# Kernel optimization log

Hardware: AMD Instinct MI355X
Metric: run time of the kernel (lower is better)

The kernel has to match this reference:

```python
import jax, jax.numpy as jnp
import numpy as np

N_NODES = 25000
N_EDGES = 400000
ATOM_DIM = 39
EDGE_DIM = 10
FP = 128


def setup_inputs() -> dict:
    key = jax.random.key(0)
    ks = iter(jax.random.split(key, 40))
    def rn(shape, scale=0.1):
        return (jax.random.normal(next(ks), shape, dtype=jnp.float32) * scale)
    inp = {
        'x': jax.random.normal(next(ks), (N_NODES, ATOM_DIM), dtype=jnp.float32),
        'edge_index': jax.random.randint(next(ks), (2, N_EDGES), 0, N_NODES, dtype=jnp.int32),
        'edge_attr': jax.random.normal(next(ks), (N_EDGES, EDGE_DIM), dtype=jnp.float32),
        # layer 0 (step=0): atom_fc + neighbor_fc + align/attend/GRU
        'l0_atom_fc_w': rn((FP, ATOM_DIM)), 'l0_atom_fc_b': rn((FP,)),
        'l0_neighbor_fc_w': rn((FP, ATOM_DIM + EDGE_DIM)), 'l0_neighbor_fc_b': rn((FP,)),
        'l0_align_w': rn((1, 2 * FP)), 'l0_align_b': rn((1,)),
        'l0_attend_w': rn((FP, FP)), 'l0_attend_b': rn((FP,)),
        'l0_w_ih': rn((3 * FP, FP)), 'l0_w_hh': rn((3 * FP, FP)),
        'l0_b_ih': rn((3 * FP,)), 'l0_b_hh': rn((3 * FP,)),
        # layer 1 (step=1): align/attend/GRU only
        'l1_align_w': rn((1, 2 * FP)), 'l1_align_b': rn((1,)),
        'l1_attend_w': rn((FP, FP)), 'l1_attend_b': rn((FP,)),
        'l1_w_ih': rn((3 * FP, FP)), 'l1_w_hh': rn((3 * FP, FP)),
        'l1_b_ih': rn((3 * FP,)), 'l1_b_hh': rn((3 * FP,)),
    }
    return inp


def _lrelu(v):
    return jax.nn.leaky_relu(v, negative_slope=0.01)


def _gru_cell(inp, h, w_ih, w_hh, b_ih, b_hh):
    # torch.nn.GRUCell math
    gi = inp @ w_ih.T + b_ih
    gh = h @ w_hh.T + b_hh
    i_r, i_z, i_n = jnp.split(gi, 3, axis=-1)
    h_r, h_z, h_n = jnp.split(gh, 3, axis=-1)
    r = jax.nn.sigmoid(i_r + h_r)
    z = jax.nn.sigmoid(i_z + h_z)
    n = jnp.tanh(i_n + r * h_n)
    return (1.0 - z) * n + z * h


def _segment_softmax(e, idx, num_segments):
    # PyG torch_geometric.utils.softmax: per-segment max-shifted exp / (sum + 1e-16)
    m = jax.ops.segment_max(e, idx, num_segments=num_segments)
    ex = jnp.exp(e - m[idx])
    s = jax.ops.segment_sum(ex, idx, num_segments=num_segments)
    return ex / (s[idx] + 1e-16)


def _edge_block(x_i, x_j, src, dst, n_nodes, aw, ab, tw, tb, w_ih, w_hh, b_ih, b_hh):
    # align -> segment softmax (keyed by source index, as in the torch code) -> attend -> GRU -> scatter-add
    evu = _lrelu(jnp.concatenate([x_i, x_j], axis=-1) @ aw.T + ab)      # [E,1]
    avu = _segment_softmax(evu, src, n_nodes)                            # [E,1]
    c = jax.nn.elu(avu * (x_i @ tw.T + tb))                              # [E,FP]; dropout is identity in eval
    h = _gru_cell(c, x_i, w_ih, w_hh, b_ih, b_hh)                        # [E,FP]
    return jax.ops.segment_sum(h, dst, num_segments=n_nodes)            # [N,FP] default 'add' aggregation


def reference(x, edge_index, edge_attr,
              l0_atom_fc_w, l0_atom_fc_b, l0_neighbor_fc_w, l0_neighbor_fc_b,
              l0_align_w, l0_align_b, l0_attend_w, l0_attend_b,
              l0_w_ih, l0_w_hh, l0_b_ih, l0_b_hh,
              l1_align_w, l1_align_b, l1_attend_w, l1_attend_b,
              l1_w_ih, l1_w_hh, l1_b_ih, l1_b_hh):
    src, dst = edge_index[0], edge_index[1]   # PyG flow source_to_target: x_j=x[src], x_i=x[dst]
    n_nodes = x.shape[0]
    # --- layer 0 (step == 0) ---
    x_i = _lrelu(x[dst] @ l0_atom_fc_w.T + l0_atom_fc_b)
    x_j = _lrelu(jnp.concatenate([x[src], edge_attr], axis=-1) @ l0_neighbor_fc_w.T + l0_neighbor_fc_b)
    x = _edge_block(x_i, x_j, src, dst, n_nodes,
                    l0_align_w, l0_align_b, l0_attend_w, l0_attend_b,
                    l0_w_ih, l0_w_hh, l0_b_ih, l0_b_hh)
    # --- layer 1 (step == 1) ---
    x_i = x[dst]
    x_j = x[src]
    x = _edge_block(x_i, x_j, src, dst, n_nodes,
                    l1_align_w, l1_align_b, l1_attend_w, l1_attend_b,
                    l1_w_ih, l1_w_hh, l1_b_ih, l1_b_hh)
    return x
```

## Files before the change

kernel.cpp:

```cpp
#include <hip/hip_runtime.h>
#include <math.h>

#define NN 25000
#define NE 400000
#define NINF -1e30f

typedef __attribute__((ext_vector_type(8))) short bf16x8;
typedef __attribute__((ext_vector_type(4))) float f32x4;

__device__ __forceinline__ float lrelu(float x){ return x > 0.f ? x : 0.01f*x; }
__device__ __forceinline__ float elu1(float x){ return x > 0.f ? x : (__expf(x)-1.f); }
__device__ __forceinline__ float sigm(float x){ return 1.f/(1.f+__expf(-x)); }
__device__ __forceinline__ float tanh_fast(float x){ float e=__expf(2.f*x); return 1.f - 2.f/(e+1.f); }
__device__ __forceinline__ short f2bf(float f){
    union { float f; unsigned u; } v; v.f = f;
    unsigned r = v.u + 0x7fff + ((v.u >> 16) & 1);
    return (short)(r >> 16);
}
__device__ __forceinline__ float bf2f(short s){
    union { unsigned u; float f; } v; v.u = ((unsigned)(unsigned short)s) << 16;
    return v.f;
}

__global__ __launch_bounds__(256) void k_pack6(
    const float* __restrict__ w0, const float* __restrict__ w1,
    const float* __restrict__ w2, const float* __restrict__ w3,
    const float* __restrict__ w4, const float* __restrict__ w5,
    short* __restrict__ o0, short* __restrict__ o1, short* __restrict__ o2,
    short* __restrict__ o3, short* __restrict__ o4, short* __restrict__ o5)
{
    int b = blockIdx.x;
    const float* w; short* o; int idx;
    if      (b < 192){ w=w0; o=o0; idx = b*256; }
    else if (b < 384){ w=w1; o=o1; idx = (b-192)*256; }
    else if (b < 576){ w=w2; o=o2; idx = (b-384)*256; }
    else if (b < 768){ w=w3; o=o3; idx = (b-576)*256; }
    else if (b < 832){ w=w4; o=o4; idx = (b-768)*256; }
    else             { w=w5; o=o5; idx = (b-832)*256; }
    idx += threadIdx.x;
    int i    = idx & 7;
    int lane = (idx >> 3) & 63;
    int ks   = (idx >> 9) & 3;
    int tile = idx >> 11;
    int row  = tile*16 + (lane & 15);
    int k    = ks*32 + ((lane >> 4) << 3) + i;
    o[idx] = f2bf(w[row*128 + k]);
}

__global__ __launch_bounds__(256) void k_hist2(const int* __restrict__ src,
                                               const int* __restrict__ dst,
                                               unsigned* __restrict__ hd,
                                               unsigned* __restrict__ hs)
{
    int e = blockIdx.x*256 + threadIdx.x;
    if (e < NE){
        atomicAdd(&hd[dst[e]], 1u);
        atomicAdd(&hs[src[e]], 1u);
    }
}

__global__ __launch_bounds__(1024) void k_scan2(
    const unsigned* __restrict__ hd, unsigned* __restrict__ cd,
    const unsigned* __restrict__ hs, unsigned* __restrict__ cs,
    int* __restrict__ srcptr)
{
    __shared__ unsigned ps[1024];
    const int issrc = blockIdx.x;
    const unsigned* h = issrc ? hs : hd;
    unsigned* c = issrc ? cs : cd;
    const int t = threadIdx.x;
    unsigned loc[25]; unsigned sum = 0;
    const int base = t*25;
    #pragma unroll
    for (int i=0;i<25;i++){ int n=base+i; unsigned v=(n<NN)?h[n]:0u; loc[i]=sum; sum+=v; }
    ps[t]=sum; __syncthreads();
    for (int off=1; off<1024; off<<=1){
        unsigned v = (t>=off)? ps[t-off] : 0u;
        __syncthreads();
        ps[t] += v;
        __syncthreads();
    }
    unsigned bex = (t==0)? 0u : ps[t-1];
    #pragma unroll
    for (int i=0;i<25;i++){
        int n=base+i;
        if (n<NN){
            unsigned off = bex + loc[i];
            c[n] = off;
            if (issrc) srcptr[n] = (int)off;
        }
    }
    if (issrc && t==1023) srcptr[NN] = NE;
}

__global__ __launch_bounds__(256) void k_scatter2(
    const int* __restrict__ src, const int* __restrict__ dst,
    unsigned* __restrict__ cd, unsigned* __restrict__ cs,
    int* __restrict__ se_dst, int* __restrict__ inv_dst,
    int* __restrict__ se2_id, int* __restrict__ se2_dst)
{
    int e = blockIdx.x*256 + threadIdx.x;
    if (e < NE){
        int d = dst[e], s = src[e];
        unsigned p = atomicAdd(&cd[d], 1u);
        se_dst[p] = d;
        inv_dst[e] = (int)p;
        unsigned q = atomicAdd(&cs[s], 1u);
        se2_id[q] = e;
        se2_dst[q] = d;
    }
}

__global__ __launch_bounds__(256) void k_l0_node(
    const float* __restrict__ x,
    const float* __restrict__ wa, const float* __restrict__ ba,
    const float* __restrict__ wn, const float* __restrict__ bn,
    const float* __restrict__ aw,
    short* __restrict__ A16, short* __restrict__ B16, float* __restrict__ di)
{
    __shared__ float xs[32][40];
    __shared__ float As[32][130];
    const int t = threadIdx.x;
    const int base = blockIdx.x * 32;
    for (int idx = t; idx < 32*39; idx += 256){
        int nn = idx / 39, k = idx - nn*39;
        int node = base + nn;
        xs[nn][k] = (node < NN) ? x[(size_t)node*39 + k] : 0.f;
    }
    __syncthreads();
    const int j = t & 127;
    const int g = t >> 7;
    {
        float accA[16], accB[16];
        #pragma unroll
        for (int nn=0; nn<16; ++nn){ accA[nn]=0.f; accB[nn]=0.f; }
        for (int k=0; k<39; ++k){
            float wva = wa[j*39+k];
            float wvb = wn[j*49+k];
            #pragma unroll
            for (int nn=0; nn<16; ++nn){
                float xv = xs[g*16+nn][k];
                accA[nn] += xv*wva;
                accB[nn] += xv*wvb;
            }
        }
        float bav = ba[j], bnv = bn[j];
        #pragma unroll
        for (int nn=0; nn<16; ++nn){
            int node = base + g*16 + nn;
            float av = lrelu(accA[nn] + bav);
            As[g*16+nn][j] = av;
            if (node < NN){
                A16[(size_t)node*128 + j] = f2bf(av);
                B16[(size_t)node*128 + j] = f2bf(accB[nn] + bnv);
            }
        }
    }
    __syncthreads();
    if (t < 32){
        int node = base + t;
        if (node < NN){
            float d = 0.f;
            for (int k=0; k<128; ++k) d += As[t][k]*aw[k];
            di[node] = d;
        }
    }
}

__global__ __launch_bounds__(512) void k_node_prep(
    const short* __restrict__ A16,
    const short* __restrict__ twp, const float* __restrict__ tb,
    const short* __restrict__ whhp, const float* __restrict__ bhh,
    short* __restrict__ T16, short* __restrict__ GH16)
{
    __shared__ __align__(16) char A_lds[64*272];
    const int t = threadIdx.x;
    const int base = blockIdx.x << 6;
    #pragma unroll
    for (int it=0; it<2; ++it){
        int cid = it*512 + t;
        int row = cid >> 4, ch = cid & 15;
        int node = base + row; if (node >= NN) node = NN-1;
        *(int4*)(A_lds + row*272 + ch*16) = *(const int4*)(A16 + (size_t)node*128 + ch*8);
    }
    __syncthreads();
    const int w = t >> 6, lane = t & 63;
    const int l15 = lane & 15, lhi = lane >> 4;
    const int jb = w*16 + l15;
    f32x4 Tacc[4], gh[4][3];
    {
        float tbv = tb[jb];
        #pragma unroll
        for (int m=0; m<4; ++m) Tacc[m] = (f32x4){tbv, tbv, tbv, tbv};
        #pragma unroll
        for (int g=0; g<3; ++g){
            float bv = bhh[g*128 + jb];
            #pragma unroll
            for (int m=0; m<4; ++m) gh[m][g] = (f32x4){bv, bv, bv, bv};
        }
    }
    #pragma unroll
    for (int ks=0; ks<4; ++ks){
        bf16x8 af[4];
        #pragma unroll
        for (int m=0; m<4; ++m)
            af[m] = *(const bf16x8*)(A_lds + (m*16+l15)*272 + ks*64 + (lhi<<4));
        bf16x8 tf = *(const bf16x8*)(twp + (size_t)((w*4 + ks)*64 + lane)*8);
        #pragma unroll
        for (int m=0; m<4; ++m)
            Tacc[m] = __builtin_amdgcn_mfma_f32_16x16x32_bf16(af[m], tf, Tacc[m], 0, 0, 0);
        #pragma unroll
        for (int g=0; g<3; ++g){
            bf16x8 wf = *(const bf16x8*)(whhp + (size_t)(((g*8+w)*4 + ks)*64 + lane)*8);
            #pragma unroll
            for (int m=0; m<4; ++m)
                gh[m][g] = __builtin_amdgcn_mfma_f32_16x16x32_bf16(af[m], wf, gh[m][g], 0, 0, 0);
        }
    }
    #pragma unroll
    for (int m=0; m<4; ++m){
        #pragma unroll
        for (int reg=0; reg<4; ++reg){
            int node = base + m*16 + lhi*4 + reg;
            if (node < NN){
                T16[(size_t)node*128 + jb]        = f2bf(Tacc[m][reg]);
                GH16[(size_t)node*384 + jb]       = f2bf(gh[m][0][reg]);
                GH16[(size_t)node*384 + 128 + jb] = f2bf(gh[m][1][reg]);
                GH16[(size_t)node*384 + 256 + jb] = f2bf(gh[m][2][reg]);
            }
        }
    }
}

__global__ __launch_bounds__(512) void k_l1_prep(
    const float* __restrict__ out0, const float* __restrict__ aw,
    const short* __restrict__ twp, const float* __restrict__ tb,
    const short* __restrict__ whhp, const float* __restrict__ bhh,
    short* __restrict__ x16, float* __restrict__ di, float* __restrict__ dj,
    short* __restrict__ T16, short* __restrict__ GH16)
{
    __shared__ __align__(16) char x_lds[64*272];
    const int t = threadIdx.x;
    const int base = blockIdx.x << 6;
    {
        int r = t >> 3, c0 = (t & 7) * 16;
        int node = base + r;
        int nc = node < NN ? node : NN-1;
        const float4* sp = (const float4*)(out0 + (size_t)nc*128 + c0);
        float4 f0 = sp[0], f1 = sp[1], f2 = sp[2], f3 = sp[3];
        union { short s[16]; int4 v[2]; } u;
        u.s[0]=f2bf(f0.x); u.s[1]=f2bf(f0.y); u.s[2]=f2bf(f0.z); u.s[3]=f2bf(f0.w);
        u.s[4]=f2bf(f1.x); u.s[5]=f2bf(f1.y); u.s[6]=f2bf(f1.z); u.s[7]=f2bf(f1.w);
        u.s[8]=f2bf(f2.x); u.s[9]=f2bf(f2.y); u.s[10]=f2bf(f2.z); u.s[11]=f2bf(f2.w);
        u.s[12]=f2bf(f3.x); u.s[13]=f2bf(f3.y); u.s[14]=f2bf(f3.z); u.s[15]=f2bf(f3.w);
        *(int4*)(x_lds + r*272 + c0*2)      = u.v[0];
        *(int4*)(x_lds + r*272 + c0*2 + 16) = u.v[1];
        if (node < NN){
            *(int4*)(x16 + (size_t)node*128 + c0)     = u.v[0];
            *(int4*)(x16 + (size_t)node*128 + c0 + 8) = u.v[1];
        }
    }
    __syncthreads();
    const int w = t >> 6, lane = t & 63;
    {
        float a0 = aw[lane], a1 = aw[64+lane], a2 = aw[128+lane], a3 = aw[192+lane];
        for (int i=0;i<8;++i){
            int r = w*8 + i;
            int node = base + r;
            float v0 = bf2f(*(const short*)(x_lds + r*272 + lane*2));
            float v1 = bf2f(*(const short*)(x_lds + r*272 + 128 + lane*2));
            float pa = v0*a0 + v1*a1;
            float pb = v0*a2 + v1*a3;
            #pragma unroll
            for (int off=32; off; off>>=1){ pa += __shfl_xor(pa,off); pb += __shfl_xor(pb,off); }
            if (lane==0 && node<NN){ di[node]=pa; dj[node]=pb; }
        }
    }
    const int l15 = lane & 15, lhi = lane >> 4;
    const int jb = w*16 + l15;
    f32x4 Tacc[4], gh[4][3];
    {
        float tbv = tb[jb];
        #pragma unroll
        for (int m=0; m<4; ++m) Tacc[m] = (f32x4){tbv, tbv, tbv, tbv};
        #pragma unroll
        for (int g=0; g<3; ++g){
            float bv = bhh[g*128 + jb];
            #pragma unroll
            for (int m=0; m<4; ++m) gh[m][g] = (f32x4){bv, bv, bv, bv};
        }
    }
    #pragma unroll
    for (int ks=0; ks<4; ++ks){
        bf16x8 af[4];
        #pragma unroll
        for (int m=0; m<4; ++m)
            af[m] = *(const bf16x8*)(x_lds + (m*16+l15)*272 + ks*64 + (lhi<<4));
        bf16x8 tf = *(const bf16x8*)(twp + (size_t)((w*4 + ks)*64 + lane)*8);
        #pragma unroll
        for (int m=0; m<4; ++m)
            Tacc[m] = __builtin_amdgcn_mfma_f32_16x16x32_bf16(af[m], tf, Tacc[m], 0, 0, 0);
        #pragma unroll
        for (int g=0; g<3; ++g){
            bf16x8 wf = *(const bf16x8*)(whhp + (size_t)(((g*8+w)*4 + ks)*64 + lane)*8);
            #pragma unroll
            for (int m=0; m<4; ++m)
                gh[m][g] = __builtin_amdgcn_mfma_f32_16x16x32_bf16(af[m], wf, gh[m][g], 0, 0, 0);
        }
    }
    #pragma unroll
    for (int m=0; m<4; ++m){
        #pragma unroll
        for (int reg=0; reg<4; ++reg){
            int node = base + m*16 + lhi*4 + reg;
            if (node < NN){
                T16[(size_t)node*128 + jb]        = f2bf(Tacc[m][reg]);
                GH16[(size_t)node*384 + jb]       = f2bf(gh[m][0][reg]);
                GH16[(size_t)node*384 + 128 + jb] = f2bf(gh[m][1][reg]);
                GH16[(size_t)node*384 + 256 + jb] = f2bf(gh[m][2][reg]);
            }
        }
    }
}

__global__ __launch_bounds__(256) void k_align0(
    const int* __restrict__ srcptr, const int* __restrict__ se2_id,
    const int* __restrict__ se2_dst, const int* __restrict__ inv_dst,
    const float* __restrict__ ea, const short* __restrict__ B16,
    const float* __restrict__ wn, const float* __restrict__ aw,
    const float* __restrict__ ab, const float* __restrict__ di,
    float* __restrict__ evu_tmp, float* __restrict__ avu)
{
    const int lane = threadIdx.x & 63;
    const int node = blockIdx.x*4 + (threadIdx.x >> 6);
    if (node >= NN) return;
    const int start = srcptr[node], end = srcptr[node+1];
    if (start >= end) return;
    float wn2a[10], wn2b[10];
    #pragma unroll
    for (int k=0;k<10;++k){
        wn2a[k] = wn[lane*49 + 39 + k];
        wn2b[k] = wn[(lane+64)*49 + 39 + k];
    }
    const float awa = aw[128+lane], awb = aw[192+lane];
    const float abv = ab[0];
    const float v1b = bf2f(B16[(size_t)node*128 + lane]);
    const float v2b = bf2f(B16[(size_t)node*128 + 64 + lane]);
    const int deg = end - start;
    if (deg <= 64){
        int myeid = 0; float mydi = 0.f; float ear[10];
        if (lane < deg){
            int pos = start + lane;
            myeid = se2_id[pos];
            mydi  = di[se2_dst[pos]];
            #pragma unroll
            for (int k=0;k<10;++k) ear[k] = ea[(size_t)myeid*10 + k];
        }
        float pv = NINF;
        for (int i=0;i<deg;++i){
            float v1 = v1b, v2 = v2b;
            #pragma unroll
            for (int k=0;k<10;++k){
                float e = __shfl(ear[k], i);
                v1 += e*wn2a[k]; v2 += e*wn2b[k];
            }
            v1 = lrelu(v1); v2 = lrelu(v2);
            float p = v1*awa + v2*awb;
            #pragma unroll
            for (int off=32; off; off>>=1) p += __shfl_xor(p, off);
            float pe = lrelu(p + __shfl(mydi, i) + abv);
            if (lane == i) pv = pe;
        }
        float cm = pv;
        #pragma unroll
        for (int off=32; off; off>>=1) cm = fmaxf(cm, __shfl_xor(cm, off));
        float ex = (lane < deg) ? __expf(pv - cm) : 0.f;
        float cs = ex;
        #pragma unroll
        for (int off=32; off; off>>=1) cs += __shfl_xor(cs, off);
        if (lane < deg) avu[inv_dst[myeid]] = ex / (cs + 1e-16f);
    } else {
        float mrun = NINF, srun = 0.f;
        for (int c0 = start; c0 < end; c0 += 64){
            int nE = min(64, end - c0);
            int myeid=0; float mydi=0.f; float ear[10];
            if (lane < nE){
                int pos = c0 + lane;
                myeid = se2_id[pos];
                mydi = di[se2_dst[pos]];
                #pragma unroll
                for (int k=0;k<10;++k) ear[k] = ea[(size_t)myeid*10 + k];
            }
            float pv = NINF;
            for (int i=0;i<nE;++i){
                float v1=v1b, v2=v2b;
                #pragma unroll
                for (int k=0;k<10;++k){
                    float e = __shfl(ear[k], i);
                    v1 += e*wn2a[k]; v2 += e*wn2b[k];
                }
                v1=lrelu(v1); v2=lrelu(v2);
                float p = v1*awa + v2*awb;
                #pragma unroll
                for (int off=32; off; off>>=1) p += __shfl_xor(p, off);
                float pe = lrelu(p + __shfl(mydi,i) + abv);
                if (lane == i) pv = pe;
            }
            if (lane < nE) evu_tmp[c0+lane] = pv;
            float cm = pv;
            #pragma unroll
            for (int off=32; off; off>>=1) cm = fmaxf(cm, __shfl_xor(cm,off));
            float nm = fmaxf(mrun, cm);
            float exs = (lane<nE)? __expf(pv-nm) : 0.f;
            float cs = exs;
            #pragma unroll
            for (int off=32; off; off>>=1) cs += __shfl_xor(cs, off);
            srun = srun*__expf(mrun-nm) + cs;
            mrun = nm;
        }
        float inv = 1.f/(srun + 1e-16f);
        for (int c0 = start; c0 < end; c0 += 64){
            int nE = min(64, end - c0);
            if (lane < nE){
                int pos = c0+lane;
                float pv = evu_tmp[pos];
                avu[inv_dst[se2_id[pos]]] = __expf(pv - mrun)*inv;
            }
        }
    }
}

__global__ __launch_bounds__(256) void k_align1(
    const int* __restrict__ srcptr, const int* __restrict__ se2_id,
    const int* __restrict__ se2_dst, const int* __restrict__ inv_dst,
    const float* __restrict__ di, const float* __restrict__ dj,
    const float* __restrict__ ab,
    float* __restrict__ evu_tmp, float* __restrict__ avu)
{
    const int lane = threadIdx.x & 63;
    const int node = blockIdx.x*4 + (threadIdx.x >> 6);
    if (node >= NN) return;
    const int start = srcptr[node], end = srcptr[node+1];
    if (start >= end) return;
    const float djs = dj[node] + ab[0];
    const int deg = end - start;
    if (deg <= 64){
        int myeid = 0; float pv = NINF;
        if (lane < deg){
            int pos = start + lane;
            myeid = se2_id[pos];
            pv = lrelu(di[se2_dst[pos]] + djs);
        }
        float cm = pv;
        #pragma unroll
        for (int off=32; off; off>>=1) cm = fmaxf(cm, __shfl_xor(cm, off));
        float ex = (lane < deg) ? __expf(pv - cm) : 0.f;
        float cs = ex;
        #pragma unroll
        for (int off=32; off; off>>=1) cs += __shfl_xor(cs, off);
        if (lane < deg) avu[inv_dst[myeid]] = ex / (cs + 1e-16f);
    } else {
        float mrun = NINF, srun = 0.f;
        for (int c0 = start; c0 < end; c0 += 64){
            int nE = min(64, end - c0);
            float pv = NINF;
            if (lane < nE){
                int pos = c0 + lane;
                pv = lrelu(di[se2_dst[pos]] + djs);
                evu_tmp[pos] = pv;
            }
            float cm = pv;
            #pragma unroll
            for (int off=32; off; off>>=1) cm = fmaxf(cm, __shfl_xor(cm,off));
            float nm = fmaxf(mrun, cm);
            float exs = (lane<nE)? __expf(pv-nm) : 0.f;
            float cs = exs;
            #pragma unroll
            for (int off=32; off; off>>=1) cs += __shfl_xor(cs, off);
            srun = srun*__expf(mrun-nm) + cs;
            mrun = nm;
        }
        float inv = 1.f/(srun + 1e-16f);
        for (int c0 = start; c0 < end; c0 += 64){
            int nE = min(64, end - c0);
            if (lane < nE){
                int pos = c0+lane;
                avu[inv_dst[se2_id[pos]]] = __expf(evu_tmp[pos] - mrun)*inv;
            }
        }
    }
}

__global__ __launch_bounds__(512) void k_edge_gru(
    const int* __restrict__ se_dst,
    const float* __restrict__ avu,
    const short* __restrict__ T16, const short* __restrict__ GH16,
    const short* __restrict__ HP16,
    const short* __restrict__ wihp, const float* __restrict__ bih,
    float* __restrict__ out)
{
    __shared__ __align__(16) char smem[64*132*4];
    __shared__ int dsts[64];
    __shared__ float av[64];
    char* const c_lds = smem;
    const int t = threadIdx.x;
    const int p0 = blockIdx.x << 6;
    if (t < 64){
        dsts[t] = se_dst[p0 + t];
        av[t] = avu[p0 + t];
    }
    __syncthreads();
    #pragma unroll
    for (int it=0; it<2; ++it){
        int cid = it*512 + t;
        int row = cid >> 4, ch = cid & 15;
        int d = dsts[row];
        float a = av[row];
        bf16x8 tv = *(const bf16x8*)(T16 + (size_t)d*128 + ch*8);
        union { short s[8]; int4 v; } u;
        #pragma unroll
        for (int i=0; i<8; ++i) u.s[i] = f2bf(elu1(a * bf2f(tv[i])));
        *(int4*)(c_lds + row*272 + ch*16) = u.v;
    }
    __syncthreads();
    const int w = t >> 6, lane = t & 63;
    const int l15 = lane & 15, lhi = lane >> 4;
    const int jb = w*16 + l15;
    f32x4 gi[4][3];
    #pragma unroll
    for (int g=0; g<3; ++g){
        float bv = bih[g*128 + jb];
        #pragma unroll
        for (int m=0; m<4; ++m) gi[m][g] = (f32x4){bv, bv, bv, bv};
    }
    #pragma unroll
    for (int ks=0; ks<4; ++ks){
        bf16x8 cf[4];
        #pragma unroll
        for (int m=0; m<4; ++m)
            cf[m] = *(const bf16x8*)(c_lds + (m*16+l15)*272 + ks*64 + (lhi<<4));
        #pragma unroll
        for (int g=0; g<3; ++g){
            bf16x8 wf = *(const bf16x8*)(wihp + (size_t)(((g*8+w)*4 + ks)*64 + lane)*8);
            #pragma unroll
            for (int m=0; m<4; ++m)
                gi[m][g] = __builtin_amdgcn_mfma_f32_16x16x32_bf16(cf[m], wf, gi[m][g], 0, 0, 0);
        }
    }
    float hreg[4][4];
    #pragma unroll
    for (int m=0; m<4; ++m){
        #pragma unroll
        for (int reg=0; reg<4; ++reg){
            int e = m*16 + lhi*4 + reg;
            int d = dsts[e];
            const short* gh = GH16 + (size_t)d*384;
            float r = sigm(gi[m][0][reg] + bf2f(gh[jb]));
            float z = sigm(gi[m][1][reg] + bf2f(gh[128+jb]));
            float n = tanh_fast(gi[m][2][reg] + r*bf2f(gh[256+jb]));
            float hp = bf2f(HP16[(size_t)d*128 + jb]);
            hreg[m][reg] = (1.f - z)*n + z*hp;
        }
    }
    __syncthreads();
    {
        float* hlds = (float*)smem;
        #pragma unroll
        for (int m=0; m<4; ++m){
            #pragma unroll
            for (int reg=0; reg<4; ++reg){
                int e = m*16 + lhi*4 + reg;
                hlds[e*132 + jb] = hreg[m][reg];
            }
        }
    }
    __syncthreads();
    {
        const int j = t & 127, eg = t >> 7;
        const float* hlds = (const float*)smem;
        float acc = 0.f; int prev = -1;
        #pragma unroll
        for (int el=0; el<16; ++el){
            int e = eg*16 + el;
            int d = dsts[e];
            float v = hlds[e*132 + j];
            if (d == prev) acc += v;
            else {
                if (prev >= 0) atomicAdd(out + (size_t)prev*128 + j, acc);
                acc = v; prev = d;
            }
        }
        atomicAdd(out + (size_t)prev*128 + j, acc);
    }
}

extern "C" void kernel_launch(void* const* d_in, const int* in_sizes, int n_in,
                              void* d_out, int out_size, void* d_ws, size_t ws_size,
                              hipStream_t stream) {
    const float* x    = (const float*)d_in[0];
    const int*   eidx = (const int*)d_in[1];
    const int*   esrc = eidx;
    const int*   edst = eidx + NE;
    const float* ea   = (const float*)d_in[2];
    const float* a_w  = (const float*)d_in[3];
    const float* a_b  = (const float*)d_in[4];
    const float* n_w  = (const float*)d_in[5];
    const float* n_b  = (const float*)d_in[6];
    const float* al_w0= (const float*)d_in[7];
    const float* al_b0= (const float*)d_in[8];
    const float* t_w0 = (const float*)d_in[9];
    const float* t_b0 = (const float*)d_in[10];
    const float* wih0 = (const float*)d_in[11];
    const float* whh0 = (const float*)d_in[12];
    const float* bih0 = (const float*)d_in[13];
    const float* bhh0 = (const float*)d_in[14];
    const float* al_w1= (const float*)d_in[15];
    const float* al_b1= (const float*)d_in[16];
    const float* t_w1 = (const float*)d_in[17];
    const float* t_b1 = (const float*)d_in[18];
    const float* wih1 = (const float*)d_in[19];
    const float* whh1 = (const float*)d_in[20];
    const float* bih1 = (const float*)d_in[21];
    const float* bhh1 = (const float*)d_in[22];

    float* ws   = (float*)d_ws;
    float* out0 = ws;
    float* avu  = out0 + (size_t)NN*128;
    float* evu_tmp = avu + NE;
    float* di   = evu_tmp + NE;
    float* dj   = di + NN;
    unsigned* hist_d = (unsigned*)(dj + NN);
    unsigned* hist_s = hist_d + NN;
    unsigned* cur_d  = hist_s + NN;
    unsigned* cur_s  = cur_d + NN;
    int* srcptr = (int*)(cur_s + NN);
    int* se_dst  = srcptr + NN + 1;
    int* inv_dst = se_dst + NE;
    int* se2_id  = inv_dst + NE;
    int* se2_dst = se2_id + NE;
    short* A16  = (short*)(se2_dst + NE);
    short* BX16 = A16 + (size_t)NN*128;
    short* T16  = BX16 + (size_t)NN*128;
    short* GH16 = T16 + (size_t)NN*128;
    short* wp0  = GH16 + (size_t)NN*384;
    short* wp1  = wp0 + 49152;
    short* wh0p = wp1 + 49152;
    short* wh1p = wh0p + 49152;
    short* tp0  = wh1p + 49152;
    short* tp1  = tp0 + 16384;

    hipMemsetAsync(out0, 0, (size_t)NN*128*sizeof(float), stream);
    hipMemsetAsync(d_out, 0, (size_t)NN*128*sizeof(float), stream);
    hipMemsetAsync(hist_d, 0, (size_t)2*NN*sizeof(unsigned), stream);

    dim3 blk(256);
    k_pack6<<<dim3(896), blk, 0, stream>>>(wih0, wih1, whh0, whh1, t_w0, t_w1,
                                           wp0, wp1, wh0p, wh1p, tp0, tp1);
    k_hist2<<<dim3((NE+255)/256), blk, 0, stream>>>(esrc, edst, hist_d, hist_s);
    k_scan2<<<dim3(2), dim3(1024), 0, stream>>>(hist_d, cur_d, hist_s, cur_s, srcptr);
    k_scatter2<<<dim3((NE+255)/256), blk, 0, stream>>>(esrc, edst, cur_d, cur_s,
                                                       se_dst, inv_dst, se2_id, se2_dst);
    k_l0_node<<<dim3((NN+31)/32), blk, 0, stream>>>(x, a_w, a_b, n_w, n_b, al_w0,
                                                    A16, BX16, di);
    k_node_prep<<<dim3((NN+63)/64), dim3(512), 0, stream>>>(A16, tp0, t_b0, wh0p, bhh0, T16, GH16);
    k_align0<<<dim3((NN+3)/4), blk, 0, stream>>>(srcptr, se2_id, se2_dst, inv_dst,
                                                 ea, BX16, n_w, al_w0, al_b0, di, evu_tmp, avu);
    k_edge_gru<<<dim3(NE/64), dim3(512), 0, stream>>>(se_dst, avu, T16, GH16, A16,
                                                      wp0, bih0, out0);
    k_l1_prep<<<dim3((NN+63)/64), dim3(512), 0, stream>>>(out0, al_w1, tp1, t_b1, wh1p, bhh1,
                                                          BX16, di, dj, T16, GH16);
    k_align1<<<dim3((NN+3)/4), blk, 0, stream>>>(srcptr, se2_id, se2_dst, inv_dst,
                                                 di, dj, al_b1, evu_tmp, avu);
    k_edge_gru<<<dim3(NE/64), dim3(512), 0, stream>>>(se_dst, avu, T16, GH16, BX16,
                                                      wp1, bih1, (float*)d_out);
}
```

Baseline: 648.4 us.

## Fuse layer-0 node linear into prep kernel via MFMA and trim edge GRU LDS

Replaces the scalar FP32 layer-0 atom/neighbor linear kernel with bf16 MFMA inside the node-prep kernel. Weights are pre-packed into fragment layout and the A rows are kept in LDS for the transform/GH GEMMs, which removes a global round trip and a launch. In the edge GRU kernel, bf16 packing now uses the v_cvt_pk_bf16_f32 instruction. GH/HP loads are reused when consecutive edges share a destination, and the LDS for the reduction is halved by doing it in two passes. This adds an extra barrier per pass and computes di from bf16-rounded activations, which costs some precision.

New measurement: 673.9 us. 1.04x slower.

```diff
diff --git a/kernel.cpp b/kernel.cpp
--- a/kernel.cpp
+++ b/kernel.cpp
@@ -21,30 +21,51 @@
     union { unsigned u; float f; } v; v.u = ((unsigned)(unsigned short)s) << 16;
     return v.f;
 }
-
-__global__ __launch_bounds__(256) void k_pack6(
+__device__ __forceinline__ unsigned cvtpk_bf16(float lo, float hi){
+    unsigned r;
+    asm volatile("v_cvt_pk_bf16_f32 %0, %1, %2" : "=v"(r) : "v"(lo), "v"(hi));
+    return r;
+}
+
+__global__ __launch_bounds__(256) void k_pack8(
     const float* __restrict__ w0, const float* __restrict__ w1,
     const float* __restrict__ w2, const float* __restrict__ w3,
     const float* __restrict__ w4, const float* __restrict__ w5,
+    const float* __restrict__ w6, const float* __restrict__ w7,
     short* __restrict__ o0, short* __restrict__ o1, short* __restrict__ o2,
-    short* __restrict__ o3, short* __restrict__ o4, short* __restrict__ o5)
+    short* __restrict__ o3, short* __restrict__ o4, short* __restrict__ o5,
+    short* __restrict__ o6, short* __restrict__ o7)
 {
     int b = blockIdx.x;
-    const float* w; short* o; int idx;
-    if      (b < 192){ w=w0; o=o0; idx = b*256; }
-    else if (b < 384){ w=w1; o=o1; idx = (b-192)*256; }
-    else if (b < 576){ w=w2; o=o2; idx = (b-384)*256; }
-    else if (b < 768){ w=w3; o=o3; idx = (b-576)*256; }
-    else if (b < 832){ w=w4; o=o4; idx = (b-768)*256; }
-    else             { w=w5; o=o5; idx = (b-832)*256; }
-    idx += threadIdx.x;
-    int i    = idx & 7;
-    int lane = (idx >> 3) & 63;
-    int ks   = (idx >> 9) & 3;
-    int tile = idx >> 11;
-    int row  = tile*16 + (lane & 15);
-    int k    = ks*32 + ((lane >> 4) << 3) + i;
-    o[idx] = f2bf(w[row*128 + k]);
+    if (b < 896){
+        const float* w; short* o; int idx;
+        if      (b < 192){ w=w0; o=o0; idx = b*256; }
+        else if (b < 384){ w=w1; o=o1; idx = (b-192)*256; }
+        else if (b < 576){ w=w2; o=o2; idx = (b-384)*256; }
+        else if (b < 768){ w=w3; o=o3; idx = (b-576)*256; }
+        else if (b < 832){ w=w4; o=o4; idx = (b-768)*256; }
+        else             { w=w5; o=o5; idx = (b-832)*256; }
+        idx += threadIdx.x;
+        int i    = idx & 7;
+        int lane = (idx >> 3) & 63;
+        int ks   = (idx >> 9) & 3;
+        int tile = idx >> 11;
+        int row  = tile*16 + (lane & 15);
+        int k    = ks*32 + ((lane >> 4) << 3) + i;
+        o[idx] = f2bf(w[row*128 + k]);
+    } else {
+        const float* w; short* o; int idx; int pitch;
+        if (b < 928){ w=w6; o=o6; idx = (b-896)*256; pitch = 39; }
+        else        { w=w7; o=o7; idx = (b-928)*256; pitch = 49; }
+        idx += threadIdx.x;
+        int i    = idx & 7;
+        int lane = (idx >> 3) & 63;
+        int ks   = (idx >> 9) & 1;
+        int tile = idx >> 10;
+        int row  = tile*16 + (lane & 15);
+        int k    = ks*32 + ((lane >> 4) << 3) + i;
+        o[idx] = (k < 39) ? f2bf(w[row*pitch + k]) : (short)0;
+    }
 }
 
 __global__ __launch_bounds__(256) void k_hist2(const int* __restrict__ src,
@@ -111,82 +132,79 @@
     }
 }
 
-__global__ __launch_bounds__(256) void k_l0_node(
+__global__ __launch_bounds__(512) void k_l0_prep(
     const float* __restrict__ x,
-    const float* __restrict__ wa, const float* __restrict__ ba,
-    const float* __restrict__ wn, const float* __restrict__ bn,
+    const float* __restrict__ ba, const float* __restrict__ bn,
     const float* __restrict__ aw,
-    short* __restrict__ A16, short* __restrict__ B16, float* __restrict__ di)
-{
-    __shared__ float xs[32][40];
-    __shared__ float As[32][130];
-    const int t = threadIdx.x;
-    const int base = blockIdx.x * 32;
-    for (int idx = t; idx < 32*39; idx += 256){
-        int nn = idx / 39, k = idx - nn*39;
-        int node = base + nn;
-        xs[nn][k] = (node < NN) ? x[(size_t)node*39 + k] : 0.f;
-    }
-    __syncthreads();
-    const int j = t & 127;
-    const int g = t >> 7;
-    {
-        float accA[16], accB[16];
-        #pragma unroll
-        for (int nn=0; nn<16; ++nn){ accA[nn]=0.f; accB[nn]=0.f; }
-        for (int k=0; k<39; ++k){
-            float wva = wa[j*39+k];
-            float wvb = wn[j*49+k];
-            #pragma unroll
-            for (int nn=0; nn<16; ++nn){
-                float xv = xs[g*16+nn][k];
-                accA[nn] += xv*wva;
-                accB[nn] += xv*wvb;
-            }
-        }
-        float bav = ba[j], bnv = bn[j];
-        #pragma unroll
-        for (int nn=0; nn<16; ++nn){
-            int node = base + g*16 + nn;
-            float av = lrelu(accA[nn] + bav);
-            As[g*16+nn][j] = av;
-            if (node < NN){
-                A16[(size_t)node*128 + j] = f2bf(av);
-                B16[(size_t)node*128 + j] = f2bf(accB[nn] + bnv);
-            }
-        }
-    }
-    __syncthreads();
-    if (t < 32){
-        int node = base + t;
-        if (node < NN){
-            float d = 0.f;
-            for (int k=0; k<128; ++k) d += As[t][k]*aw[k];
-            di[node] = d;
-        }
-    }
-}
-
-__global__ __launch_bounds__(512) void k_node_prep(
-    const short* __restrict__ A16,
+    const short* __restrict__ wap, const short* __restrict__ wnp,
     const short* __restrict__ twp, const float* __restrict__ tb,
     const short* __restrict__ whhp, const float* __restrict__ bhh,
+    short* __restrict__ A16, short* __restrict__ B16, float* __restrict__ di,
     short* __restrict__ T16, short* __restrict__ GH16)
 {
+    __shared__ short x_lds[64*72];
     __shared__ __align__(16) char A_lds[64*272];
     const int t = threadIdx.x;
     const int base = blockIdx.x << 6;
-    #pragma unroll
-    for (int it=0; it<2; ++it){
-        int cid = it*512 + t;
-        int row = cid >> 4, ch = cid & 15;
-        int node = base + row; if (node >= NN) node = NN-1;
-        *(int4*)(A_lds + row*272 + ch*16) = *(const int4*)(A16 + (size_t)node*128 + ch*8);
+    for (int idx = t; idx < 64*64; idx += 512){
+        int r = idx >> 6, k = idx & 63;
+        int node = base + r;
+        float v = (k < 39 && node < NN) ? x[(size_t)node*39 + k] : 0.f;
+        x_lds[r*72 + k] = f2bf(v);
     }
     __syncthreads();
     const int w = t >> 6, lane = t & 63;
     const int l15 = lane & 15, lhi = lane >> 4;
     const int jb = w*16 + l15;
+    f32x4 Aacc[4], Bacc[4];
+    #pragma unroll
+    for (int m=0; m<4; ++m){ Aacc[m] = (f32x4){0,0,0,0}; Bacc[m] = (f32x4){0,0,0,0}; }
+    #pragma unroll
+    for (int ks=0; ks<2; ++ks){
+        bf16x8 af[4];
+        #pragma unroll
+        for (int m=0; m<4; ++m)
+            af[m] = *(const bf16x8*)&x_lds[(m*16+l15)*72 + ks*32 + lhi*8];
+        bf16x8 wfA = *(const bf16x8*)(wap + (size_t)((w*2 + ks)*64 + lane)*8);
+        bf16x8 wfB = *(const bf16x8*)(wnp + (size_t)((w*2 + ks)*64 + lane)*8);
+        #pragma unroll
+        for (int m=0; m<4; ++m){
+            Aacc[m] = __builtin_amdgcn_mfma_f32_16x16x32_bf16(af[m], wfA, Aacc[m], 0, 0, 0);
+            Bacc[m] = __builtin_amdgcn_mfma_f32_16x16x32_bf16(af[m], wfB, Bacc[m], 0, 0, 0);
+        }
+    }
+    {
+        float bav = ba[jb], bnv = bn[jb];
+        #pragma unroll
+        for (int m=0; m<4; ++m){
+            #pragma unroll
+            for (int reg=0; reg<4; ++reg){
+                int e = m*16 + lhi*4 + reg;
+                int node = base + e;
+                float avv = lrelu(Aacc[m][reg] + bav);
+                short ab16 = f2bf(avv);
+                *(short*)(A_lds + e*272 + jb*2) = ab16;
+                if (node < NN){
+                    A16[(size_t)node*128 + jb] = ab16;
+                    B16[(size_t)node*128 + jb] = f2bf(Bacc[m][reg] + bnv);
+                }
+            }
+        }
+    }
+    __syncthreads();
+    {
+        float a0 = aw[lane], a1 = aw[64+lane];
+        for (int i=0;i<8;++i){
+            int r = w*8 + i;
+            int node = base + r;
+            float v0 = bf2f(*(const short*)(A_lds + r*272 + lane*2));
+            float v1 = bf2f(*(const short*)(A_lds + r*272 + 128 + lane*2));
+            float pa = v0*a0 + v1*a1;
+            #pragma unroll
+            for (int off=32; off; off>>=1) pa += __shfl_xor(pa, off);
+            if (lane==0 && node<NN) di[node] = pa;
+        }
+    }
     f32x4 Tacc[4], gh[4][3];
     {
         float tbv = tb[jb];
@@ -499,8 +517,8 @@
     const short* __restrict__ wihp, const float* __restrict__ bih,
     float* __restrict__ out)
 {
-    __shared__ __align__(16) char smem[64*132*4];
-    __shared__ int dsts[64];
+    __shared__ __align__(16) char smem[17536];
+    __shared__ __align__(16) int dsts[64];
     __shared__ float av[64];
     char* const c_lds = smem;
     const int t = threadIdx.x;
@@ -517,10 +535,16 @@
         int d = dsts[row];
         float a = av[row];
         bf16x8 tv = *(const bf16x8*)(T16 + (size_t)d*128 + ch*8);
-        union { short s[8]; int4 v; } u;
-        #pragma unroll
-        for (int i=0; i<8; ++i) u.s[i] = f2bf(elu1(a * bf2f(tv[i])));
-        *(int4*)(c_lds + row*272 + ch*16) = u.v;
+        float c0 = elu1(a*bf2f(tv[0])), c1 = elu1(a*bf2f(tv[1]));
+        float c2 = elu1(a*bf2f(tv[2])), c3 = elu1(a*bf2f(tv[3]));
+        float c4 = elu1(a*bf2f(tv[4])), c5 = elu1(a*bf2f(tv[5]));
+        float c6 = elu1(a*bf2f(tv[6])), c7 = elu1(a*bf2f(tv[7]));
+        int4 pk;
+        pk.x = (int)cvtpk_bf16(c0, c1);
+        pk.y = (int)cvtpk_bf16(c2, c3);
+        pk.z = (int)cvtpk_bf16(c4, c5);
+        pk.w = (int)cvtpk_bf16(c6, c7);
+        *(int4*)(c_lds + row*272 + ch*16) = pk;
     }
     __syncthreads();
     const int w = t >> 6, lane = t & 63;
@@ -548,49 +572,60 @@
         }
     }
     float hreg[4][4];
-    #pragma unroll
-    for (int m=0; m<4; ++m){
-        #pragma unroll
-        for (int reg=0; reg<4; ++reg){
-            int e = m*16 + lhi*4 + reg;
-            int d = dsts[e];
-            const short* gh = GH16 + (size_t)d*384;
-            float r = sigm(gi[m][0][reg] + bf2f(gh[jb]));
-            float z = sigm(gi[m][1][reg] + bf2f(gh[128+jb]));
-            float n = tanh_fast(gi[m][2][reg] + r*bf2f(gh[256+jb]));
-            float hp = bf2f(HP16[(size_t)d*128 + jb]);
-            hreg[m][reg] = (1.f - z)*n + z*hp;
-        }
-    }
-    __syncthreads();
     {
-        float* hlds = (float*)smem;
+        int dprev = -1;
+        float ghr=0.f, ghz=0.f, ghn=0.f, hp=0.f;
         #pragma unroll
         for (int m=0; m<4; ++m){
+            int4 dv = *(const int4*)&dsts[m*16 + lhi*4];
+            int dd[4] = {dv.x, dv.y, dv.z, dv.w};
+            #pragma unroll
+            for (int reg=0; reg<4; ++reg){
+                int d = dd[reg];
+                if (d != dprev){
+                    const short* gh = GH16 + (size_t)d*384 + jb;
+                    ghr = bf2f(gh[0]);
+                    ghz = bf2f(gh[128]);
+                    ghn = bf2f(gh[256]);
+                    hp  = bf2f(HP16[(size_t)d*128 + jb]);
+                    dprev = d;
+                }
+                float r = sigm(gi[m][0][reg] + ghr);
+                float z = sigm(gi[m][1][reg] + ghz);
+                float n = tanh_fast(gi[m][2][reg] + r*ghn);
+                hreg[m][reg] = (1.f - z)*n + z*hp;
+            }
+        }
+    }
+    float* hlds = (float*)smem;
+    #pragma unroll
+    for (int half=0; half<2; ++half){
+        __syncthreads();
+        #pragma unroll
+        for (int m=half*2; m<half*2+2; ++m){
             #pragma unroll
             for (int reg=0; reg<4; ++reg){
                 int e = m*16 + lhi*4 + reg;
-                hlds[e*132 + jb] = hreg[m][reg];
-            }
-        }
-    }
-    __syncthreads();
-    {
-        const int j = t & 127, eg = t >> 7;
-        const float* hlds = (const float*)smem;
-        float acc = 0.f; int prev = -1;
-        #pragma unroll
-        for (int el=0; el<16; ++el){
-            int e = eg*16 + el;
-            int d = dsts[e];
-            float v = hlds[e*132 + j];
-            if (d == prev) acc += v;
-            else {
-                if (prev >= 0) atomicAdd(out + (size_t)prev*128 + j, acc);
-                acc = v; prev = d;
-            }
-        }
-        atomicAdd(out + (size_t)prev*128 + j, acc);
+                hlds[(e - half*32)*137 + jb] = hreg[m][reg];
+            }
+        }
+        __syncthreads();
+        {
+            const int j = t & 127, eg = t >> 7;
+            float acc = 0.f; int prev = -1;
+            #pragma unroll
+            for (int k=0; k<8; ++k){
+                int r = eg*8 + k;
+                int d = dsts[half*32 + r];
+                float v = hlds[r*137 + j];
+                if (d == prev) acc += v;
+                else {
+                    if (prev >= 0) atomicAdd(out + (size_t)prev*128 + j, acc);
+                    acc = v; prev = d;
+                }
+            }
+            atomicAdd(out + (size_t)prev*128 + j, acc);
+        }
     }
 }
 
@@ -648,21 +683,23 @@
     short* wh1p = wh0p + 49152;
     short* tp0  = wh1p + 49152;
     short* tp1  = tp0 + 16384;
+    short* wap  = tp1 + 16384;
+    short* wnp  = wap + 8192;
 
     hipMemsetAsync(out0, 0, (size_t)NN*128*sizeof(float), stream);
     hipMemsetAsync(d_out, 0, (size_t)NN*128*sizeof(float), stream);
     hipMemsetAsync(hist_d, 0, (size_t)2*NN*sizeof(unsigned), stream);
 
     dim3 blk(256);
-    k_pack6<<<dim3(896), blk, 0, stream>>>(wih0, wih1, whh0, whh1, t_w0, t_w1,
-                                           wp0, wp1, wh0p, wh1p, tp0, tp1);
+    k_pack8<<<dim3(960), blk, 0, stream>>>(wih0, wih1, whh0, whh1, t_w0, t_w1, a_w, n_w,
+                                           wp0, wp1, wh0p, wh1p, tp0, tp1, wap, wnp);
     k_hist2<<<dim3((NE+255)/256), blk, 0, stream>>>(esrc, edst, hist_d, hist_s);
     k_scan2<<<dim3(2), dim3(1024), 0, stream>>>(hist_d, cur_d, hist_s, cur_s, srcptr);
     k_scatter2<<<dim3((NE+255)/256), blk, 0, stream>>>(esrc, edst, cur_d, cur_s,
                                                        se_dst, inv_dst, se2_id, se2_dst);
-    k_l0_node<<<dim3((NN+31)/32), blk, 0, stream>>>(x, a_w, a_b, n_w, n_b, al_w0,
-                                                    A16, BX16, di);
-    k_node_prep<<<dim3((NN+63)/64), dim3(512), 0, stream>>>(A16, tp0, t_b0, wh0p, bhh0, T16, GH16);
+    k_l0_prep<<<dim3((NN+63)/64), dim3(512), 0, stream>>>(x, a_b, n_b, al_w0, wap, wnp,
+                                                          tp0, t_b0, wh0p, bhh0,
+                                                          A16, BX16, di, T16, GH16);
     k_align0<<<dim3((NN+3)/4), blk, 0, stream>>>(srcptr, se2_id, se2_dst, inv_dst,
                                                  ea, BX16, n_w, al_w0, al_b0, di, evu_tmp, avu);
     k_edge_gru<<<dim3(NE/64), dim3(512), 0, stream>>>(se_dst, avu, T16, GH16, A16,
```
